# Optimization experiments

Measured on AMD Instinct MI355X. Metric: run time of the kernel, lower is better.

Reference implementation:

```python
import jax, jax.numpy as jnp
import numpy as np

N = 20000      # nodes (spots)
D = 256        # embed_dim
H = 4          # n_heads
DH = D // H    # head dim
L = 2          # n_layers
E = 320000     # edges (avg degree 16)
K = 48         # static padded-neighbor cap (>= true max degree for this data)
EPS = 1e-5
NEG = -1e30


def setup_inputs() -> dict:
    key = jax.random.key(0)
    ks = jax.random.split(key, 8)
    s = 0.05
    return {
        "expr_embed": jax.random.normal(ks[0], (N, D), jnp.float32),
        "spatial_embed": jax.random.normal(ks[1], (N, D), jnp.float32),
        "in_proj_w": jax.random.normal(ks[2], (L, 3 * D, D), jnp.float32) * s,
        "in_proj_b": jnp.zeros((L, 3 * D), jnp.float32),
        "out_proj_w": jax.random.normal(ks[3], (L, D, D), jnp.float32) * s,
        "out_proj_b": jnp.zeros((L, D), jnp.float32),
        "ffn_w1": jax.random.normal(ks[4], (L, 2 * D, D), jnp.float32) * s,
        "ffn_b1": jnp.zeros((L, 2 * D), jnp.float32),
        "ffn_w2": jax.random.normal(ks[5], (L, D, 2 * D), jnp.float32) * s,
        "ffn_b2": jnp.zeros((L, D), jnp.float32),
        "ln1_g": jnp.ones((L, D), jnp.float32),
        "ln1_b": jnp.zeros((L, D), jnp.float32),
        "ln2_g": jnp.ones((L, D), jnp.float32),
        "ln2_b": jnp.zeros((L, D), jnp.float32),
        "edge_index": jax.random.randint(ks[6], (2, E), 0, N, jnp.int32),
    }


def _build_neighbors(edge_index):
    """Padded neighbor indices (N,K) and key_padding_mask (N,K) (True = pad)."""
    src, tgt = edge_index[0], edge_index[1]
    counts = jnp.zeros((N,), jnp.int32).at[tgt].add(1)
    order = jnp.argsort(tgt)                       # group edges by target
    src_s, tgt_s = src[order], tgt[order]
    offsets = jnp.concatenate([jnp.zeros((1,), jnp.int32),
                               jnp.cumsum(counts)[:-1].astype(jnp.int32)])
    pos = jnp.arange(E, dtype=jnp.int32) - offsets[tgt_s]
    pos = jnp.where(pos < K, pos, K)               # K is out-of-bounds -> dropped
    nbr = jnp.zeros((N, K), jnp.int32).at[tgt_s, pos].set(src_s, mode='drop')
    pad = jnp.ones((N, K), bool).at[tgt_s, pos].set(False, mode='drop')
    iso = counts == 0                              # isolated spots attend to self
    nbr = nbr.at[:, 0].set(jnp.where(iso, jnp.arange(N, dtype=jnp.int32), nbr[:, 0]))
    pad = pad.at[:, 0].set(jnp.where(iso, False, pad[:, 0]))
    return nbr, pad


def _layernorm(x, g, b):
    mu = jnp.mean(x, -1, keepdims=True)
    var = jnp.var(x, -1, keepdims=True)
    return (x - mu) * jax.lax.rsqrt(var + EPS) * g + b


def _forward(expr_embed, spatial_embed, in_proj_w, in_proj_b, out_proj_w,
             out_proj_b, ffn_w1, ffn_b1, ffn_w2, ffn_b2,
             ln1_g, ln1_b, ln2_g, ln2_b, nbr, pad):
    x = expr_embed
    scale = 1.0 / jnp.sqrt(jnp.asarray(DH, x.dtype))
    for i in range(L):
        Wq, Wk, Wv = jnp.split(in_proj_w[i], 3, axis=0)
        bq, bk, bv = jnp.split(in_proj_b[i], 3, axis=0)
        q = (x @ Wq.T + bq).reshape(N, H, DH)
        # project spatial once, gather projected rows (same math as gather-then-project)
        k = (spatial_embed @ Wk.T + bk)[nbr].reshape(N, K, H, DH)
        v = (spatial_embed @ Wv.T + bv)[nbr].reshape(N, K, H, DH)
        scores = jnp.einsum('nhd,nkhd->nhk', q, k) * scale      # (N,H,K)
        scores = jnp.where(pad[:, None, :], NEG, scores)
        attn = jax.nn.softmax(scores, axis=-1)
        ao = jnp.einsum('nhk,nkhd->nhd', attn, v).reshape(N, D)
        ao = ao @ out_proj_w[i].T + out_proj_b[i]
        x = _layernorm(x + ao, ln1_g[i], ln1_b[i])
        h = jax.nn.gelu(x @ ffn_w1[i].T + ffn_b1[i], approximate=False)
        h = h @ ffn_w2[i].T + ffn_b2[i]
        x = _layernorm(x + h, ln2_g[i], ln2_b[i])
    return x


def reference(expr_embed, spatial_embed, in_proj_w, in_proj_b, out_proj_w,
              out_proj_b, ffn_w1, ffn_b1, ffn_w2, ffn_b2,
              ln1_g, ln1_b, ln2_g, ln2_b, edge_index):
    nbr, pad = _build_neighbors(edge_index.astype(jnp.int32))
    return _forward(expr_embed, spatial_embed, in_proj_w, in_proj_b, out_proj_w,
                    out_proj_b, ffn_w1, ffn_b1, ffn_w2, ffn_b2,
                    ln1_g, ln1_b, ln2_g, ln2_b, nbr, pad)
```

## Files before the change

kernel.cpp:

```cpp
#include <hip/hip_runtime.h>

#define N_NODES 20000
#define DIM 256
#define NHEAD 4
#define DHEAD 64
#define NLAYER 2
#define NEDGE 320000
#define KCAP 48
#define NBM64 313

typedef __bf16 v8bf __attribute__((ext_vector_type(8)));
typedef float v4f __attribute__((ext_vector_type(4)));

union LU { uint4 u; v8bf v; };

__device__ __forceinline__ unsigned short f2bf(float f) {
    unsigned u = __float_as_uint(f);
    unsigned r = u + 0x7FFFu + ((u >> 16) & 1u);
    return (unsigned short)(r >> 16);
}
__device__ __forceinline__ float bflo(unsigned u) { return __uint_as_float(u << 16); }
__device__ __forceinline__ float bfhi(unsigned u) { return __uint_as_float(u & 0xFFFF0000u); }

__global__ void sniff_kernel(const unsigned short* __restrict__ p,
                             int* __restrict__ flag) {
    __shared__ int s;
    if (threadIdx.x == 0) s = 0;
    __syncthreads();
    int c = 0;
    for (int i = threadIdx.x; i < 4096; i += 256) {
        unsigned short u = p[i];
        unsigned e = (u >> 7) & 0xFFu;
        if (e == 0xFFu) c++;
        else if (e == 0u && (u & 0x7Fu)) c++;
    }
    atomicAdd(&s, c);
    __syncthreads();
    if (threadIdx.x == 0) flag[0] = (s >= 4) ? 1 : 0;
}

struct ConvBfArgs { const void* src[6]; unsigned short* dst[6]; int n[6]; };

__global__ void conv_bf16_kernel(ConvBfArgs a, const int* __restrict__ flag) {
    const int t  = blockIdx.y;
    const int n  = a.n[t];
    const int i0 = (blockIdx.x * 256 + threadIdx.x) * 4;
    if (i0 >= n) return;
    unsigned short* dst = a.dst[t];
    if (flag[0]) {
        float4 v = *(const float4*)((const float*)a.src[t] + i0);
        ushort4 o;
        o.x = f2bf(v.x); o.y = f2bf(v.y); o.z = f2bf(v.z); o.w = f2bf(v.w);
        *(ushort4*)(dst + i0) = o;
    } else {
        ushort4 u = *(const ushort4*)((const unsigned short*)a.src[t] + i0);
        *(ushort4*)(dst + i0) = u;
    }
}

struct ConvF32Args { const void* src[8]; float* dst[8]; int n[8]; };

__global__ void conv_f32_kernel(ConvF32Args a, const int* __restrict__ flag) {
    const int t  = blockIdx.y;
    const int n  = a.n[t];
    const int i0 = (blockIdx.x * 256 + threadIdx.x) * 4;
    if (i0 >= n) return;
    float* dst = a.dst[t];
    if (flag[0]) {
        float4 v = *(const float4*)((const float*)a.src[t] + i0);
        *(float4*)(dst + i0) = v;
    } else {
        ushort4 u = *(const ushort4*)((const unsigned short*)a.src[t] + i0);
        *(float4*)(dst + i0) = make_float4(bflo(u.x), bflo(u.y), bflo(u.z), bflo(u.w));
    }
}

__global__ void zero_cnt_kernel(int* __restrict__ cnt) {
    int i = blockIdx.x * 256 + threadIdx.x;
    if (i < N_NODES) cnt[i] = 0;
}

__global__ void build_nbr_kernel(const int* __restrict__ ei,
                                 int* __restrict__ cnt, int* __restrict__ nbr) {
    int e = blockIdx.x * 256 + threadIdx.x;
    if (e >= NEDGE) return;
    int s = ei[e];
    int t = ei[NEDGE + e];
    int slot = atomicAdd(&cnt[t], 1);
    if (slot < KCAP) nbr[t * KCAP + slot] = s;
}

__device__ __forceinline__ void gemm_body(
    __bf16 (*As)[72], __bf16 (*Bs)[72],
    const unsigned short* __restrict__ A, const unsigned short* __restrict__ B,
    const float* __restrict__ bias, unsigned short* __restrict__ C,
    int M, int Nc, int Kd, int m0, int nB, int nC, int do_gelu)
{
    const int tid  = threadIdx.x;
    const int wave = tid >> 6;
    const int lane = tid & 63;
    const int wn0  = wave * 32;
    const int lm   = lane & 15;
    const int lk   = (lane >> 4) * 8;
    const int srow = tid >> 3;
    const int scol = (tid & 7) << 3;

    uint4 pa[2], pb[4];
#pragma unroll
    for (int i = 0; i < 2; ++i) {
        int row = srow + i * 32;
        pa[i] = make_uint4(0u, 0u, 0u, 0u);
        if (m0 + row < M)
            pa[i] = *(const uint4*)&A[(size_t)(m0 + row) * Kd + scol];
    }
#pragma unroll
    for (int i = 0; i < 4; ++i) {
        int row = srow + i * 32;
        pb[i] = *(const uint4*)&B[(size_t)(nB + row) * Kd + scol];
    }

    v4f acc[4][2] = {};

    for (int k0 = 0; k0 < Kd; k0 += 64) {
#pragma unroll
        for (int i = 0; i < 2; ++i) { LU t; t.u = pa[i]; *(v8bf*)&As[srow + i * 32][scol] = t.v; }
#pragma unroll
        for (int i = 0; i < 4; ++i) { LU t; t.u = pb[i]; *(v8bf*)&Bs[srow + i * 32][scol] = t.v; }
        __syncthreads();

        const int kn = k0 + 64;
        if (kn < Kd) {
#pragma unroll
            for (int i = 0; i < 2; ++i) {
                int row = srow + i * 32;
                pa[i] = make_uint4(0u, 0u, 0u, 0u);
                if (m0 + row < M)
                    pa[i] = *(const uint4*)&A[(size_t)(m0 + row) * Kd + kn + scol];
            }
#pragma unroll
            for (int i = 0; i < 4; ++i) {
                int row = srow + i * 32;
                pb[i] = *(const uint4*)&B[(size_t)(nB + row) * Kd + kn + scol];
            }
        }

#pragma unroll
        for (int ks = 0; ks < 2; ++ks) {
            v8bf af[4], bq[2];
#pragma unroll
            for (int mi = 0; mi < 4; ++mi)
                af[mi] = *(const v8bf*)&As[mi * 16 + lm][ks * 32 + lk];
#pragma unroll
            for (int ni = 0; ni < 2; ++ni)
                bq[ni] = *(const v8bf*)&Bs[wn0 + ni * 16 + lm][ks * 32 + lk];
#pragma unroll
            for (int mi = 0; mi < 4; ++mi)
#pragma unroll
                for (int ni = 0; ni < 2; ++ni)
                    acc[mi][ni] = __builtin_amdgcn_mfma_f32_16x16x32_bf16(
                        af[mi], bq[ni], acc[mi][ni], 0, 0, 0);
        }
        __syncthreads();
    }

    const int rq = (lane >> 4) << 2;
#pragma unroll
    for (int ni = 0; ni < 2; ++ni) {
        int colb = wn0 + ni * 16 + lm;
        float bv = bias[nB + colb];
        int colc = nC + colb;
#pragma unroll
        for (int mi = 0; mi < 4; ++mi) {
#pragma unroll
            for (int r = 0; r < 4; ++r) {
                int row = m0 + mi * 16 + rq + r;
                if (row >= M) continue;
                float v = acc[mi][ni][r] + bv;
                if (do_gelu) v = 0.5f * v * (1.0f + erff(v * 0.7071067811865475f));
                C[(size_t)row * Nc + colc] = f2bf(v);
            }
        }
    }
}

__global__ __launch_bounds__(256) void gemm_kernel(
    const unsigned short* __restrict__ A, const unsigned short* __restrict__ B,
    const float* __restrict__ bias, unsigned short* __restrict__ C,
    int M, int Nc, int Kd, int do_gelu)
{
    __shared__ __align__(16) __bf16 As[64][72];
    __shared__ __align__(16) __bf16 Bs[128][72];
    const int n0 = blockIdx.y * 128;
    gemm_body(As, Bs, A, B, bias, C, M, Nc, Kd, blockIdx.x * 64, n0, n0, do_gelu);
}

__global__ __launch_bounds__(256) void qkv_kernel(
    const unsigned short* __restrict__ x, const unsigned short* __restrict__ spat,
    const unsigned short* __restrict__ W, const float* __restrict__ bias,
    unsigned short* __restrict__ q, unsigned short* __restrict__ kv, int M)
{
    __shared__ __align__(16) __bf16 As[64][72];
    __shared__ __align__(16) __bf16 Bs[128][72];
    const int y = blockIdx.y;
    const unsigned short* A = (y < 2) ? x : spat;
    unsigned short*       C = (y < 2) ? q : kv;
    const int Nc = (y < 2) ? 256 : 512;
    const int nB = y * 128;
    const int nC = (y < 2) ? nB : nB - 256;
    gemm_body(As, Bs, A, W, bias, C, M, Nc, 256, blockIdx.x * 64, nB, nC, 0);
}

__global__ __launch_bounds__(256) void attn_kernel(
    const unsigned short* __restrict__ q,
    const unsigned short* __restrict__ kv,
    const int* __restrict__ nbr,
    const int* __restrict__ cnt,
    unsigned short* __restrict__ ao)
{
    const int n    = blockIdx.x;
    const int tid  = threadIdx.x;
    const int h    = tid >> 6;
    const int lane = tid & 63;

    __shared__ float sc[NHEAD][KCAP];
    __shared__ int   nbs[KCAP];

    int deg = cnt[n];
    if (deg > KCAP) deg = KCAP;
    const bool iso = (deg == 0);
    if (iso) deg = 1;

    if (tid < KCAP)
        nbs[tid] = (tid < deg) ? (iso ? n : nbr[n * KCAP + tid]) : 0;
    __syncthreads();

    {
        const int sub = lane & 7;
        const int grp = lane >> 3;
        float qf[8];
        {
            uint4 qu = *(const uint4*)&q[(size_t)n * DIM + h * DHEAD + sub * 8];
            qf[0] = bflo(qu.x); qf[1] = bfhi(qu.x);
            qf[2] = bflo(qu.y); qf[3] = bfhi(qu.y);
            qf[4] = bflo(qu.z); qf[5] = bfhi(qu.z);
            qf[6] = bflo(qu.w); qf[7] = bfhi(qu.w);
        }
        const int nit = (deg + 7) >> 3;
        for (int it = 0; it < nit; ++it) {
            int j  = it * 8 + grp;
            int jc = (j < deg) ? j : (deg - 1);
            int nb = nbs[jc];
            uint4 ku = *(const uint4*)&kv[(size_t)nb * 512 + h * DHEAD + sub * 8];
            float p = qf[0] * bflo(ku.x);
            p = fmaf(qf[1], bfhi(ku.x), p);
            p = fmaf(qf[2], bflo(ku.y), p);
            p = fmaf(qf[3], bfhi(ku.y), p);
            p = fmaf(qf[4], bflo(ku.z), p);
            p = fmaf(qf[5], bfhi(ku.z), p);
            p = fmaf(qf[6], bflo(ku.w), p);
            p = fmaf(qf[7], bfhi(ku.w), p);
            p += __shfl_xor(p, 1, 64);
            p += __shfl_xor(p, 2, 64);
            p += __shfl_xor(p, 4, 64);
            if (sub == 0 && j < deg) sc[h][j] = p * 0.125f;
        }
    }
    __syncthreads();

    {
        float s  = (lane < deg) ? sc[h][lane] : -1e30f;
        float mx = s;
#pragma unroll
        for (int m = 32; m >= 1; m >>= 1) mx = fmaxf(mx, __shfl_xor(mx, m, 64));
        float e   = (lane < deg) ? __expf(s - mx) : 0.0f;
        float sum = e;
#pragma unroll
        for (int m = 32; m >= 1; m >>= 1) sum += __shfl_xor(sum, m, 64);
        float inv = 1.0f / sum;
        if (lane < KCAP) sc[h][lane] = e * inv;
    }
    __syncthreads();

    {
        const int quarter = lane >> 4;
        const int d0      = (lane & 15) * 4;
        float a0 = 0.f, a1 = 0.f, a2 = 0.f, a3 = 0.f;
        for (int j = 0; j < deg; j += 4) {
            int j0 = j + quarter;
            int jc = (j0 < deg) ? j0 : (deg - 1);
            int nb = nbs[jc];
            uint2 u = *(const uint2*)&kv[(size_t)nb * 512 + 256 + h * DHEAD + d0];
            float w = (j0 < deg) ? sc[h][j0] : 0.f;
            a0 = fmaf(w, bflo(u.x), a0);
            a1 = fmaf(w, bfhi(u.x), a1);
            a2 = fmaf(w, bflo(u.y), a2);
            a3 = fmaf(w, bfhi(u.y), a3);
        }
        a0 += __shfl_xor(a0, 16, 64); a0 += __shfl_xor(a0, 32, 64);
        a1 += __shfl_xor(a1, 16, 64); a1 += __shfl_xor(a1, 32, 64);
        a2 += __shfl_xor(a2, 16, 64); a2 += __shfl_xor(a2, 32, 64);
        a3 += __shfl_xor(a3, 16, 64); a3 += __shfl_xor(a3, 32, 64);
        if (lane < 16) {
            uint2 o;
            o.x = (unsigned)f2bf(a0) | ((unsigned)f2bf(a1) << 16);
            o.y = (unsigned)f2bf(a2) | ((unsigned)f2bf(a3) << 16);
            *(uint2*)&ao[(size_t)n * DIM + h * DHEAD + d0] = o;
        }
    }
}

__global__ __launch_bounds__(256) void ln_add_kernel(
    const unsigned short* __restrict__ x, const unsigned short* __restrict__ t,
    const float* __restrict__ g, const float* __restrict__ b,
    unsigned short* __restrict__ xout, void* __restrict__ dout,
    int final_out, const int* __restrict__ flag)
{
    const int wave = threadIdx.x >> 6;
    const int lane = threadIdx.x & 63;
    const int row  = blockIdx.x * 4 + wave;

    const ushort4 xu = *(const ushort4*)&x[(size_t)row * DIM + lane * 4];
    const ushort4 tu = *(const ushort4*)&t[(size_t)row * DIM + lane * 4];
    float v[4];
    v[0] = bflo(xu.x) + bflo(tu.x);
    v[1] = bflo(xu.y) + bflo(tu.y);
    v[2] = bflo(xu.z) + bflo(tu.z);
    v[3] = bflo(xu.w) + bflo(tu.w);

    float s = 0.f, ss = 0.f;
#pragma unroll
    for (int i = 0; i < 4; ++i) { s += v[i]; ss += v[i] * v[i]; }
#pragma unroll
    for (int m = 32; m >= 1; m >>= 1) {
        s  += __shfl_xor(s, m, 64);
        ss += __shfl_xor(ss, m, 64);
    }
    const float mu  = s * (1.0f / DIM);
    const float var = ss * (1.0f / DIM) - mu * mu;
    const float r   = rsqrtf(var + 1e-5f);

    float o[4];
#pragma unroll
    for (int i = 0; i < 4; ++i) {
        int c = lane * 4 + i;
        o[i] = (v[i] - mu) * r * g[c] + b[c];
    }
    if (final_out) {
        if (flag[0]) {
            *(float4*)&((float*)dout)[(size_t)row * DIM + lane * 4] =
                make_float4(o[0], o[1], o[2], o[3]);
        } else {
            ushort4 u;
            u.x = f2bf(o[0]); u.y = f2bf(o[1]); u.z = f2bf(o[2]); u.w = f2bf(o[3]);
            *(ushort4*)&((unsigned short*)dout)[(size_t)row * DIM + lane * 4] = u;
        }
    } else {
        ushort4 u;
        u.x = f2bf(o[0]); u.y = f2bf(o[1]); u.z = f2bf(o[2]); u.w = f2bf(o[3]);
        *(ushort4*)&xout[(size_t)row * DIM + lane * 4] = u;
    }
}

extern "C" void kernel_launch(void* const* d_in, const int* in_sizes, int n_in,
                              void* d_out, int out_size, void* d_ws, size_t ws_size,
                              hipStream_t stream) {
    const int* ei = (const int*)d_in[14];

    char* ws = (char*)d_ws;
    size_t off = 0;
    auto alloc = [&](size_t bytes) -> void* {
        void* p = ws + off;
        off = (off + bytes + 255) & ~(size_t)255;
        return p;
    };

    const int bidx[6] = { 0, 1, 2, 4, 6, 8 };
    const int bnn[6]  = { N_NODES * DIM, N_NODES * DIM,
                          NLAYER * 3 * DIM * DIM, NLAYER * DIM * DIM,
                          NLAYER * 2 * DIM * DIM, NLAYER * DIM * 2 * DIM };
    ConvBfArgs cb;
    unsigned short* canb[6];
    for (int i = 0; i < 6; ++i) {
        canb[i] = (unsigned short*)alloc((size_t)bnn[i] * 2);
        cb.src[i] = d_in[bidx[i]];
        cb.dst[i] = canb[i];
        cb.n[i]   = bnn[i];
    }
    const unsigned short* expr_b = canb[0];
    const unsigned short* spat_b = canb[1];
    const unsigned short* ipw    = canb[2];
    const unsigned short* opw    = canb[3];
    const unsigned short* w1     = canb[4];
    const unsigned short* w2     = canb[5];

    const int fidx[8] = { 3, 5, 7, 9, 10, 11, 12, 13 };
    const int fn[8]   = { NLAYER * 3 * DIM, NLAYER * DIM, NLAYER * 2 * DIM,
                          NLAYER * DIM, NLAYER * DIM, NLAYER * DIM,
                          NLAYER * DIM, NLAYER * DIM };
    ConvF32Args cf;
    float* canf[8];
    for (int i = 0; i < 8; ++i) {
        canf[i] = (float*)alloc((size_t)fn[i] * 4);
        cf.src[i] = d_in[fidx[i]];
        cf.dst[i] = canf[i];
        cf.n[i]   = fn[i];
    }

    unsigned short* x_buf  = (unsigned short*)alloc((size_t)N_NODES * DIM * 2);
    unsigned short* q_buf  = (unsigned short*)alloc((size_t)N_NODES * DIM * 2);
    unsigned short* kv_buf = (unsigned short*)alloc((size_t)N_NODES * 2 * DIM * 2);
    unsigned short* ao_buf = (unsigned short*)alloc((size_t)N_NODES * DIM * 2);
    unsigned short* h_buf  = (unsigned short*)alloc((size_t)N_NODES * 2 * DIM * 2);
    unsigned short* t_buf  = (unsigned short*)alloc((size_t)N_NODES * DIM * 2);
    int* cnt  = (int*)alloc((size_t)N_NODES * 4);
    int* nbr  = (int*)alloc((size_t)N_NODES * KCAP * 4);
    int* flag = (int*)alloc(256);

    sniff_kernel<<<1, 256, 0, stream>>>((const unsigned short*)d_in[0], flag);
    conv_bf16_kernel<<<dim3((N_NODES * DIM) / 1024, 6), 256, 0, stream>>>(cb, flag);
    conv_f32_kernel<<<dim3(2, 8), 256, 0, stream>>>(cf, flag);
    zero_cnt_kernel<<<(N_NODES + 255) / 256, 256, 0, stream>>>(cnt);
    build_nbr_kernel<<<(NEDGE + 255) / 256, 256, 0, stream>>>(ei, cnt, nbr);

    for (int i = 0; i < NLAYER; ++i) {
        const unsigned short* Wqkv = ipw + (size_t)i * 3 * DIM * DIM;
        const float*          bqkv = canf[0] + (size_t)i * 3 * DIM;
        const unsigned short* xin  = (i == 0) ? expr_b : x_buf;

        qkv_kernel<<<dim3(NBM64, 6), 256, 0, stream>>>(
            xin, spat_b, Wqkv, bqkv, q_buf, kv_buf, N_NODES);
        attn_kernel<<<N_NODES, 256, 0, stream>>>(q_buf, kv_buf, nbr, cnt, ao_buf);
        gemm_kernel<<<dim3(NBM64, 2), 256, 0, stream>>>(
            ao_buf, opw + (size_t)i * DIM * DIM, canf[1] + (size_t)i * DIM,
            t_buf, N_NODES, DIM, DIM, 0);
        ln_add_kernel<<<N_NODES / 4, 256, 0, stream>>>(
            xin, t_buf, canf[4] + (size_t)i * DIM, canf[5] + (size_t)i * DIM,
            x_buf, nullptr, 0, flag);
        gemm_kernel<<<dim3(NBM64, 4), 256, 0, stream>>>(
            x_buf, w1 + (size_t)i * 2 * DIM * DIM, canf[2] + (size_t)i * 2 * DIM,
            h_buf, N_NODES, 2 * DIM, DIM, 1);
        gemm_kernel<<<dim3(NBM64, 2), 256, 0, stream>>>(
            h_buf, w2 + (size_t)i * DIM * 2 * DIM, canf[3] + (size_t)i * DIM,
            t_buf, N_NODES, DIM, 2 * DIM, 0);
        ln_add_kernel<<<N_NODES / 4, 256, 0, stream>>>(
            x_buf, t_buf, canf[6] + (size_t)i * DIM, canf[7] + (size_t)i * DIM,
            x_buf, d_out, (i == NLAYER - 1) ? 1 : 0, flag);
    }
}
```

Before: 449.4 us.

## Fuse out-proj and FFN2 GEMMs with residual LayerNorm; trim attention syncs

Adds a GEMM kernel whose block covers a full 256-wide row tile. It adds bias and residual, computes LayerNorm statistics across waves through shared memory, and writes the normalized result directly. This replaces the gemm_kernel + ln_add_kernel pairs and drops the t_buf round trip and four launches. The attention kernel now keeps a neighbor-index copy per wave, so its block barriers can go. It also uses bf16 fdot2 for the QK dot products and drops the index clamps by relying on zero padding. The count-zeroing kernel is merged into the sniff kernel. In exchange, the fused GEMM launches half as many blocks, and its epilogue uses scalar 2-byte stores.

New measurement: 440.2 us. 2.0% less time.

```diff
diff --git a/kernel.cpp b/kernel.cpp
--- a/kernel.cpp
+++ b/kernel.cpp
@@ -10,9 +10,11 @@
 #define NBM64 313
 
 typedef __bf16 v8bf __attribute__((ext_vector_type(8)));
+typedef __bf16 v2bf __attribute__((ext_vector_type(2)));
 typedef float v4f __attribute__((ext_vector_type(4)));
 
-union LU { uint4 u; v8bf v; };
+union LU  { uint4 u; v8bf v; };
+union U32 { unsigned u; v2bf v; };
 
 __device__ __forceinline__ unsigned short f2bf(float f) {
     unsigned u = __float_as_uint(f);
@@ -22,21 +24,26 @@
 __device__ __forceinline__ float bflo(unsigned u) { return __uint_as_float(u << 16); }
 __device__ __forceinline__ float bfhi(unsigned u) { return __uint_as_float(u & 0xFFFF0000u); }
 
-__global__ void sniff_kernel(const unsigned short* __restrict__ p,
-                             int* __restrict__ flag) {
-    __shared__ int s;
-    if (threadIdx.x == 0) s = 0;
-    __syncthreads();
-    int c = 0;
-    for (int i = threadIdx.x; i < 4096; i += 256) {
-        unsigned short u = p[i];
-        unsigned e = (u >> 7) & 0xFFu;
-        if (e == 0xFFu) c++;
-        else if (e == 0u && (u & 0x7Fu)) c++;
-    }
-    atomicAdd(&s, c);
-    __syncthreads();
-    if (threadIdx.x == 0) flag[0] = (s >= 4) ? 1 : 0;
+__global__ void sniffzero_kernel(const unsigned short* __restrict__ p,
+                                 int* __restrict__ flag, int* __restrict__ cnt) {
+    if (blockIdx.x == 0) {
+        __shared__ int s;
+        if (threadIdx.x == 0) s = 0;
+        __syncthreads();
+        int c = 0;
+        for (int i = threadIdx.x; i < 4096; i += 256) {
+            unsigned short u = p[i];
+            unsigned e = (u >> 7) & 0xFFu;
+            if (e == 0xFFu) c++;
+            else if (e == 0u && (u & 0x7Fu)) c++;
+        }
+        atomicAdd(&s, c);
+        __syncthreads();
+        if (threadIdx.x == 0) flag[0] = (s >= 4) ? 1 : 0;
+    } else {
+        int i = (blockIdx.x - 1) * 256 + threadIdx.x;
+        if (i < N_NODES) cnt[i] = 0;
+    }
 }
 
 struct ConvBfArgs { const void* src[6]; unsigned short* dst[6]; int n[6]; };
@@ -75,11 +82,6 @@
     }
 }
 
-__global__ void zero_cnt_kernel(int* __restrict__ cnt) {
-    int i = blockIdx.x * 256 + threadIdx.x;
-    if (i < N_NODES) cnt[i] = 0;
-}
-
 __global__ void build_nbr_kernel(const int* __restrict__ ei,
                                  int* __restrict__ cnt, int* __restrict__ nbr) {
     int e = blockIdx.x * 256 + threadIdx.x;
@@ -210,6 +212,167 @@
     gemm_body(As, Bs, A, W, bias, C, M, Nc, 256, blockIdx.x * 64, nB, nC, 0);
 }
 
+__global__ __launch_bounds__(256) void gemm_ln_kernel(
+    const unsigned short* __restrict__ A, const unsigned short* __restrict__ B,
+    const float* __restrict__ bias, const unsigned short* __restrict__ xres,
+    const float* __restrict__ g, const float* __restrict__ bb,
+    unsigned short* __restrict__ xout, void* __restrict__ dout,
+    int M, int Kd, int final_out, const int* __restrict__ flag)
+{
+    __shared__ __align__(16) __bf16 As[64][72];
+    __shared__ __align__(16) __bf16 Bs[256][72];
+    __shared__ float partS[4][64], partSS[4][64];
+    __shared__ float totMu[64], totR[64];
+
+    const int tid  = threadIdx.x;
+    const int m0   = blockIdx.x * 64;
+    const int wave = tid >> 6;
+    const int lane = tid & 63;
+    const int wn0  = wave * 64;
+    const int lm   = lane & 15;
+    const int lk   = (lane >> 4) * 8;
+    const int srow = tid >> 3;
+    const int scol = (tid & 7) << 3;
+
+    uint4 pa[2], pb[8];
+#pragma unroll
+    for (int i = 0; i < 2; ++i) {
+        int row = srow + i * 32;
+        pa[i] = make_uint4(0u, 0u, 0u, 0u);
+        if (m0 + row < M)
+            pa[i] = *(const uint4*)&A[(size_t)(m0 + row) * Kd + scol];
+    }
+#pragma unroll
+    for (int i = 0; i < 8; ++i) {
+        int row = srow + i * 32;
+        pb[i] = *(const uint4*)&B[(size_t)row * Kd + scol];
+    }
+
+    v4f acc[4][4] = {};
+
+    for (int k0 = 0; k0 < Kd; k0 += 64) {
+#pragma unroll
+        for (int i = 0; i < 2; ++i) { LU t; t.u = pa[i]; *(v8bf*)&As[srow + i * 32][scol] = t.v; }
+#pragma unroll
+        for (int i = 0; i < 8; ++i) { LU t; t.u = pb[i]; *(v8bf*)&Bs[srow + i * 32][scol] = t.v; }
+        __syncthreads();
+
+        const int kn = k0 + 64;
+        if (kn < Kd) {
+#pragma unroll
+            for (int i = 0; i < 2; ++i) {
+                int row = srow + i * 32;
+                pa[i] = make_uint4(0u, 0u, 0u, 0u);
+                if (m0 + row < M)
+                    pa[i] = *(const uint4*)&A[(size_t)(m0 + row) * Kd + kn + scol];
+            }
+#pragma unroll
+            for (int i = 0; i < 8; ++i) {
+                int row = srow + i * 32;
+                pb[i] = *(const uint4*)&B[(size_t)row * Kd + kn + scol];
+            }
+        }
+
+#pragma unroll
+        for (int ks = 0; ks < 2; ++ks) {
+            v8bf af[4], bq[4];
+#pragma unroll
+            for (int mi = 0; mi < 4; ++mi)
+                af[mi] = *(const v8bf*)&As[mi * 16 + lm][ks * 32 + lk];
+#pragma unroll
+            for (int ni = 0; ni < 4; ++ni)
+                bq[ni] = *(const v8bf*)&Bs[wn0 + ni * 16 + lm][ks * 32 + lk];
+#pragma unroll
+            for (int mi = 0; mi < 4; ++mi)
+#pragma unroll
+                for (int ni = 0; ni < 4; ++ni)
+                    acc[mi][ni] = __builtin_amdgcn_mfma_f32_16x16x32_bf16(
+                        af[mi], bq[ni], acc[mi][ni], 0, 0, 0);
+        }
+        __syncthreads();
+    }
+
+    const int rq = (lane >> 4) << 2;
+    float gv[4], bv2[4], biasv[4];
+#pragma unroll
+    for (int ni = 0; ni < 4; ++ni) {
+        int col = wn0 + ni * 16 + lm;
+        biasv[ni] = bias[col];
+        gv[ni]    = g[col];
+        bv2[ni]   = bb[col];
+    }
+
+    float sl[4][4] = {}, ssl[4][4] = {};
+#pragma unroll
+    for (int mi = 0; mi < 4; ++mi) {
+#pragma unroll
+        for (int r = 0; r < 4; ++r) {
+            int row = m0 + mi * 16 + rq + r;
+#pragma unroll
+            for (int ni = 0; ni < 4; ++ni) {
+                int col = wn0 + ni * 16 + lm;
+                float resv = bflo((unsigned)xres[(size_t)row * DIM + col]);
+                float v = acc[mi][ni][r] + biasv[ni] + resv;
+                acc[mi][ni][r] = v;
+                sl[mi][r]  += v;
+                ssl[mi][r] += v * v;
+            }
+        }
+    }
+#pragma unroll
+    for (int mi = 0; mi < 4; ++mi)
+#pragma unroll
+        for (int r = 0; r < 4; ++r) {
+#pragma unroll
+            for (int m = 1; m <= 8; m <<= 1) {
+                sl[mi][r]  += __shfl_xor(sl[mi][r],  m, 64);
+                ssl[mi][r] += __shfl_xor(ssl[mi][r], m, 64);
+            }
+        }
+    if (lm == 0) {
+#pragma unroll
+        for (int mi = 0; mi < 4; ++mi)
+#pragma unroll
+            for (int r = 0; r < 4; ++r) {
+                partS[wave][mi * 16 + rq + r]  = sl[mi][r];
+                partSS[wave][mi * 16 + rq + r] = ssl[mi][r];
+            }
+    }
+    __syncthreads();
+    if (tid < 64) {
+        float S = partS[0][tid] + partS[1][tid] + partS[2][tid] + partS[3][tid];
+        float SS = partSS[0][tid] + partSS[1][tid] + partSS[2][tid] + partSS[3][tid];
+        float mu  = S * (1.0f / DIM);
+        float var = SS * (1.0f / DIM) - mu * mu;
+        totMu[tid] = mu;
+        totR[tid]  = rsqrtf(var + 1e-5f);
+    }
+    __syncthreads();
+
+#pragma unroll
+    for (int mi = 0; mi < 4; ++mi) {
+#pragma unroll
+        for (int r = 0; r < 4; ++r) {
+            int lrow = mi * 16 + rq + r;
+            int row  = m0 + lrow;
+            if (row >= M) continue;
+            float mu = totMu[lrow];
+            float rv = totR[lrow];
+#pragma unroll
+            for (int ni = 0; ni < 4; ++ni) {
+                int col = wn0 + ni * 16 + lm;
+                float o = (acc[mi][ni][r] - mu) * rv * gv[ni] + bv2[ni];
+                if (final_out) {
+                    if (flag[0]) ((float*)dout)[(size_t)row * DIM + col] = o;
+                    else ((unsigned short*)dout)[(size_t)row * DIM + col] = f2bf(o);
+                } else {
+                    xout[(size_t)row * DIM + col] = f2bf(o);
+                }
+            }
+        }
+    }
+}
+
 __global__ __launch_bounds__(256) void attn_kernel(
     const unsigned short* __restrict__ q,
     const unsigned short* __restrict__ kv,
@@ -223,49 +386,49 @@
     const int lane = tid & 63;
 
     __shared__ float sc[NHEAD][KCAP];
-    __shared__ int   nbs[KCAP];
+    __shared__ int   nbs[NHEAD][KCAP];
 
     int deg = cnt[n];
     if (deg > KCAP) deg = KCAP;
     const bool iso = (deg == 0);
     if (iso) deg = 1;
 
-    if (tid < KCAP)
-        nbs[tid] = (tid < deg) ? (iso ? n : nbr[n * KCAP + tid]) : 0;
-    __syncthreads();
+    if (lane < KCAP)
+        nbs[h][lane] = (lane < deg) ? (iso ? n : nbr[n * KCAP + lane]) : 0;
 
     {
         const int sub = lane & 7;
         const int grp = lane >> 3;
-        float qf[8];
-        {
-            uint4 qu = *(const uint4*)&q[(size_t)n * DIM + h * DHEAD + sub * 8];
-            qf[0] = bflo(qu.x); qf[1] = bfhi(qu.x);
-            qf[2] = bflo(qu.y); qf[3] = bfhi(qu.y);
-            qf[4] = bflo(qu.z); qf[5] = bfhi(qu.z);
-            qf[6] = bflo(qu.w); qf[7] = bfhi(qu.w);
-        }
+        const uint4 qu = *(const uint4*)&q[(size_t)n * DIM + h * DHEAD + sub * 8];
+        const unsigned short* kbase = kv + h * DHEAD + sub * 8;
         const int nit = (deg + 7) >> 3;
         for (int it = 0; it < nit; ++it) {
             int j  = it * 8 + grp;
-            int jc = (j < deg) ? j : (deg - 1);
-            int nb = nbs[jc];
-            uint4 ku = *(const uint4*)&kv[(size_t)nb * 512 + h * DHEAD + sub * 8];
-            float p = qf[0] * bflo(ku.x);
-            p = fmaf(qf[1], bfhi(ku.x), p);
-            p = fmaf(qf[2], bflo(ku.y), p);
-            p = fmaf(qf[3], bfhi(ku.y), p);
-            p = fmaf(qf[4], bflo(ku.z), p);
-            p = fmaf(qf[5], bfhi(ku.z), p);
-            p = fmaf(qf[6], bflo(ku.w), p);
-            p = fmaf(qf[7], bfhi(ku.w), p);
+            int nb = nbs[h][j];
+            uint4 ku = *(const uint4*)&kbase[(size_t)nb * 512];
+#if __has_builtin(__builtin_amdgcn_fdot2_f32_bf16)
+            U32 a0{qu.x}, a1{qu.y}, a2{qu.z}, a3{qu.w};
+            U32 b0{ku.x}, b1{ku.y}, b2{ku.z}, b3{ku.w};
+            float p = __builtin_amdgcn_fdot2_f32_bf16(a0.v, b0.v, 0.0f, false);
+            p = __builtin_amdgcn_fdot2_f32_bf16(a1.v, b1.v, p, false);
+            p = __builtin_amdgcn_fdot2_f32_bf16(a2.v, b2.v, p, false);
+            p = __builtin_amdgcn_fdot2_f32_bf16(a3.v, b3.v, p, false);
+#else
+            float p = bflo(qu.x) * bflo(ku.x);
+            p = fmaf(bfhi(qu.x), bfhi(ku.x), p);
+            p = fmaf(bflo(qu.y), bflo(ku.y), p);
+            p = fmaf(bfhi(qu.y), bfhi(ku.y), p);
+            p = fmaf(bflo(qu.z), bflo(ku.z), p);
+            p = fmaf(bfhi(qu.z), bfhi(ku.z), p);
+            p = fmaf(bflo(qu.w), bflo(ku.w), p);
+            p = fmaf(bfhi(qu.w), bfhi(ku.w), p);
+#endif
             p += __shfl_xor(p, 1, 64);
             p += __shfl_xor(p, 2, 64);
             p += __shfl_xor(p, 4, 64);
             if (sub == 0 && j < deg) sc[h][j] = p * 0.125f;
         }
     }
-    __syncthreads();
 
     {
         float s  = (lane < deg) ? sc[h][lane] : -1e30f;
@@ -279,18 +442,18 @@
         float inv = 1.0f / sum;
         if (lane < KCAP) sc[h][lane] = e * inv;
     }
-    __syncthreads();
 
     {
         const int quarter = lane >> 4;
         const int d0      = (lane & 15) * 4;
+        const unsigned short* vbase = kv + 256 + h * DHEAD + d0;
+        const int dmax = (deg + 3) & ~3;
         float a0 = 0.f, a1 = 0.f, a2 = 0.f, a3 = 0.f;
-        for (int j = 0; j < deg; j += 4) {
+        for (int j = 0; j < dmax; j += 4) {
             int j0 = j + quarter;
-            int jc = (j0 < deg) ? j0 : (deg - 1);
-            int nb = nbs[jc];
-            uint2 u = *(const uint2*)&kv[(size_t)nb * 512 + 256 + h * DHEAD + d0];
-            float w = (j0 < deg) ? sc[h][j0] : 0.f;
+            int nb = nbs[h][j0];
+            uint2 u = *(const uint2*)&vbase[(size_t)nb * 512];
+            float w = sc[h][j0];
             a0 = fmaf(w, bflo(u.x), a0);
             a1 = fmaf(w, bfhi(u.x), a1);
             a2 = fmaf(w, bflo(u.y), a2);
@@ -306,58 +469,6 @@
             o.y = (unsigned)f2bf(a2) | ((unsigned)f2bf(a3) << 16);
             *(uint2*)&ao[(size_t)n * DIM + h * DHEAD + d0] = o;
         }
-    }
-}
-
-__global__ __launch_bounds__(256) void ln_add_kernel(
-    const unsigned short* __restrict__ x, const unsigned short* __restrict__ t,
-    const float* __restrict__ g, const float* __restrict__ b,
-    unsigned short* __restrict__ xout, void* __restrict__ dout,
-    int final_out, const int* __restrict__ flag)
-{
-    const int wave = threadIdx.x >> 6;
-    const int lane = threadIdx.x & 63;
-    const int row  = blockIdx.x * 4 + wave;
-
-    const ushort4 xu = *(const ushort4*)&x[(size_t)row * DIM + lane * 4];
-    const ushort4 tu = *(const ushort4*)&t[(size_t)row * DIM + lane * 4];
-    float v[4];
-    v[0] = bflo(xu.x) + bflo(tu.x);
-    v[1] = bflo(xu.y) + bflo(tu.y);
-    v[2] = bflo(xu.z) + bflo(tu.z);
-    v[3] = bflo(xu.w) + bflo(tu.w);
-
-    float s = 0.f, ss = 0.f;
-#pragma unroll
-    for (int i = 0; i < 4; ++i) { s += v[i]; ss += v[i] * v[i]; }
-#pragma unroll
-    for (int m = 32; m >= 1; m >>= 1) {
-        s  += __shfl_xor(s, m, 64);
-        ss += __shfl_xor(ss, m, 64);
-    }
-    const float mu  = s * (1.0f / DIM);
-    const float var = ss * (1.0f / DIM) - mu * mu;
-    const float r   = rsqrtf(var + 1e-5f);
-
-    float o[4];
-#pragma unroll
-    for (int i = 0; i < 4; ++i) {
-        int c = lane * 4 + i;
-        o[i] = (v[i] - mu) * r * g[c] + b[c];
-    }
-    if (final_out) {
-        if (flag[0]) {
-            *(float4*)&((float*)dout)[(size_t)row * DIM + lane * 4] =
-                make_float4(o[0], o[1], o[2], o[3]);
-        } else {
-            ushort4 u;
-            u.x = f2bf(o[0]); u.y = f2bf(o[1]); u.z = f2bf(o[2]); u.w = f2bf(o[3]);
-            *(ushort4*)&((unsigned short*)dout)[(size_t)row * DIM + lane * 4] = u;
-        }
-    } else {
-        ushort4 u;
-        u.x = f2bf(o[0]); u.y = f2bf(o[1]); u.z = f2bf(o[2]); u.w = f2bf(o[3]);
-        *(ushort4*)&xout[(size_t)row * DIM + lane * 4] = u;
     }
 }
 
@@ -411,15 +522,14 @@
     unsigned short* kv_buf = (unsigned short*)alloc((size_t)N_NODES * 2 * DIM * 2);
     unsigned short* ao_buf = (unsigned short*)alloc((size_t)N_NODES * DIM * 2);
     unsigned short* h_buf  = (unsigned short*)alloc((size_t)N_NODES * 2 * DIM * 2);
-    unsigned short* t_buf  = (unsigned short*)alloc((size_t)N_NODES * DIM * 2);
     int* cnt  = (int*)alloc((size_t)N_NODES * 4);
     int* nbr  = (int*)alloc((size_t)N_NODES * KCAP * 4);
     int* flag = (int*)alloc(256);
 
-    sniff_kernel<<<1, 256, 0, stream>>>((const unsigned short*)d_in[0], flag);
+    sniffzero_kernel<<<1 + (N_NODES + 255) / 256, 256, 0, stream>>>(
+        (const unsigned short*)d_in[0], flag, cnt);
     conv_bf16_kernel<<<dim3((N_NODES * DIM) / 1024, 6), 256, 0, stream>>>(cb, flag);
     conv_f32_kernel<<<dim3(2, 8), 256, 0, stream>>>(cf, flag);
-    zero_cnt_kernel<<<(N_NODES + 255) / 256, 256, 0, stream>>>(cnt);
     build_nbr_kernel<<<(NEDGE + 255) / 256, 256, 0, stream>>>(ei, cnt, nbr);
 
     for (int i = 0; i < NLAYER; ++i) {
@@ -430,20 +540,16 @@
         qkv_kernel<<<dim3(NBM64, 6), 256, 0, stream>>>(
             xin, spat_b, Wqkv, bqkv, q_buf, kv_buf, N_NODES);
         attn_kernel<<<N_NODES, 256, 0, stream>>>(q_buf, kv_buf, nbr, cnt, ao_buf);
-        gemm_kernel<<<dim3(NBM64, 2), 256, 0, stream>>>(
+        gemm_ln_kernel<<<NBM64, 256, 0, stream>>>(
             ao_buf, opw + (size_t)i * DIM * DIM, canf[1] + (size_t)i * DIM,
-            t_buf, N_NODES, DIM, DIM, 0);
-        ln_add_kernel<<<N_NODES / 4, 256, 0, stream>>>(
-            xin, t_buf, canf[4] + (size_t)i * DIM, canf[5] + (size_t)i * DIM,
-            x_buf, nullptr, 0, flag);
+            xin, canf[4] + (size_t)i * DIM, canf[5] + (size_t)i * DIM,
+            x_buf, nullptr, N_NODES, DIM, 0, flag);
         gemm_kernel<<<dim3(NBM64, 4), 256, 0, stream>>>(
             x_buf, w1 + (size_t)i * 2 * DIM * DIM, canf[2] + (size_t)i * 2 * DIM,
             h_buf, N_NODES, 2 * DIM, DIM, 1);
-        gemm_kernel<<<dim3(NBM64, 2), 256, 0, stream>>>(
+        gemm_ln_kernel<<<NBM64, 256, 0, stream>>>(
             h_buf, w2 + (size_t)i * DIM * 2 * DIM, canf[3] + (size_t)i * DIM,
-            t_buf, N_NODES, DIM, 2 * DIM, 0);
-        ln_add_kernel<<<N_NODES / 4, 256, 0, stream>>>(
-            x_buf, t_buf, canf[6] + (size_t)i * DIM, canf[7] + (size_t)i * DIM,
-            x_buf, d_out, (i == NLAYER - 1) ? 1 : 0, flag);
-    }
-}
+            x_buf, canf[6] + (size_t)i * DIM, canf[7] + (size_t)i * DIM,
+            x_buf, d_out, N_NODES, 2 * DIM, (i == NLAYER - 1) ? 1 : 0, flag);
+    }
+}
```
